# Performance work log

Measured on AMD Instinct MI355X. Metric: run time of the kernel, lower is better.

## Reference

```python
import jax, jax.numpy as jnp
import numpy as np

NUM_ORI = 16
DEGREE = 2
NUM_LAYERS = 2
LN_EPS = 1e-6


def ori_grid_s1(n):
    theta = jnp.linspace(0.0, 2.0 * jnp.pi, n + 1)[:-1]
    return jnp.stack([jnp.cos(theta), jnp.sin(theta)], axis=-1)  # (O, 2)


def poly_feats(z, degree):
    # PolynomialFeatures: [z, z*z outer, (z*z)*z outer ...] flattened
    feats = [z]
    p = z
    for _ in range(degree):
        p = (p[..., :, None] * z[..., None, :]).reshape(*z.shape[:-1], -1)
        feats.append(p)
    return jnp.concatenate(feats, axis=-1)


def basis_mlp(z, W1, b1, W2, b2):
    return jax.nn.gelu(jax.nn.gelu(z @ W1 + b1) @ W2 + b2)


def layer_norm(h, scale, bias):
    mu = h.mean(axis=-1, keepdims=True)
    var = ((h - mu) ** 2).mean(axis=-1, keepdims=True)
    return (h - mu) * jax.lax.rsqrt(var + LN_EPS) * scale + bias


def setup_inputs() -> dict:
    key = jax.random.key(0)
    ks = jax.random.split(key, 16)
    B, N, NIN, H, BD, WF, OUT, L = 1, 256, 3, 64, 32, 4, 3, NUM_LAYERS
    s = 0.05
    return {
        'pos': jax.random.normal(ks[0], (B, N, 2), jnp.float32),
        'x': jax.random.normal(ks[1], (B, N, NIN), jnp.float32),
        'skb_W1': jax.random.normal(ks[2], (14, H), jnp.float32) * s,
        'skb_b1': jnp.zeros((H,), jnp.float32),
        'skb_W2': jax.random.normal(ks[3], (H, BD), jnp.float32) * s,
        'skb_b2': jnp.zeros((BD,), jnp.float32),
        'rkb_W1': jax.random.normal(ks[4], (3, H), jnp.float32) * s,
        'rkb_b1': jnp.zeros((H,), jnp.float32),
        'rkb_W2': jax.random.normal(ks[5], (H, BD), jnp.float32) * s,
        'rkb_b2': jnp.zeros((BD,), jnp.float32),
        'emb_W': jax.random.normal(ks[6], (NIN, H), jnp.float32) * s,
        'conv_sW': jax.random.normal(ks[7], (L, BD, H), jnp.float32) * s,
        'conv_rW': jax.random.normal(ks[8], (L, BD, H), jnp.float32) * s,
        'conv_b': jnp.zeros((L, H), jnp.float32),
        'ln_scale': jnp.ones((L, H), jnp.float32),
        'ln_bias': jnp.zeros((L, H), jnp.float32),
        'lin1_W': jax.random.normal(ks[9], (L, H, WF * H), jnp.float32) * s,
        'lin1_b': jnp.zeros((L, WF * H), jnp.float32),
        'lin2_W': jax.random.normal(ks[10], (L, WF * H, H), jnp.float32) * s,
        'lin2_b': jnp.zeros((L, H), jnp.float32),
        'readout_W': jax.random.normal(ks[11], (H, OUT), jnp.float32) * s,
    }


def reference(pos, x, skb_W1, skb_b1, skb_W2, skb_b2, rkb_W1, rkb_b1, rkb_W2, rkb_b2,
              emb_W, conv_sW, conv_rW, conv_b, ln_scale, ln_bias,
              lin1_W, lin1_b, lin2_W, lin2_b, readout_W):
    ori = ori_grid_s1(NUM_ORI)  # (O, 2)
    # rel_pos: (B, n, m, 1, 2) -> broadcast against ori (O, 2)
    rel_pos = pos[:, None, :, None, :] - pos[:, :, None, None, :]
    inv1 = jnp.sum(rel_pos * ori[None, None, None, :, :], axis=-1, keepdims=True)  # (B,N,N,O,1)
    inv2 = jnp.linalg.norm(rel_pos - rel_pos * inv1, axis=-1, keepdims=True)       # (B,N,N,O,1)
    spatial_inv = jnp.concatenate([inv1, inv2], axis=-1)                            # (B,N,N,O,2)
    orient_inv = jnp.sum(ori[:, None, :] * ori[None, :, :], axis=-1, keepdims=True) # (O,O,1)

    kernel_basis = basis_mlp(poly_feats(spatial_inv, DEGREE), skb_W1, skb_b1, skb_W2, skb_b2)  # (B,N,N,O,BD)
    fiber_basis = basis_mlp(poly_feats(orient_inv, DEGREE), rkb_W1, rkb_b1, rkb_W2, rkb_b2)    # (O,O,BD)

    h = x @ emb_W                                  # (B,N,H)
    O = NUM_ORI
    h = jnp.broadcast_to(h[:, :, None, :], (h.shape[0], h.shape[1], O, h.shape[2]))  # (B,N,O,H)

    for i in range(NUM_LAYERS):
        inp = h
        sk = kernel_basis @ conv_sW[i]             # (B,N,N,O,H)
        rk = fiber_basis @ conv_rW[i]              # (O,O,H)
        c = jnp.einsum('bnoc,bmnoc->bmoc', h, sk)  # spatial aggregation
        c = jnp.einsum('bmoc,poc->bmpc', c, rk)    # orientation mixing
        c = c + conv_b[i]
        c = layer_norm(c, ln_scale[i], ln_bias[i])
        c = jax.nn.gelu(c @ lin1_W[i] + lin1_b[i]) @ lin2_W[i] + lin2_b[i]
        h = inp + c

    readout = h @ readout_W                        # (B,N,O,OUT)
    out_scalar = readout.mean(axis=-2)             # (B,N,OUT)
    out_scalar = jnp.sum(out_scalar, axis=1) / out_scalar.shape[1]  # global pool -> (B,OUT)
    return out_scalar
```

## Files before the change

kernel.cpp:

```cpp
#include <hip/hip_runtime.h>
#include <math.h>

#define NPTS 256
#define NORI 16
#define CH   64
#define BD   32
#define HID  64
#define STEP16 0.39269908169872414f

typedef __bf16 bf16x8 __attribute__((ext_vector_type(8)));
typedef float  f32x4  __attribute__((ext_vector_type(4)));

#define MFMA16(a, b, cc) __builtin_amdgcn_mfma_f32_16x16x32_bf16(a, b, cc, 0, 0, 0)

__device__ __forceinline__ float gelu_f(float x) {
    float x2 = x * x;
    float y2 = x * fmaf(0.07135481627f, x2, 1.5957691216f);
    float e = __expf(y2);
    return x - x * __builtin_amdgcn_rcpf(e + 1.0f);
}

__device__ __forceinline__ unsigned pk2(float x, float y) {
    union { __bf16 h[2]; unsigned u; } r;
    r.h[0] = (__bf16)x; r.h[1] = (__bf16)y;
    return r.u;
}

__device__ __forceinline__ void dev_prep(
    const float* __restrict__ skb_W1, const float* __restrict__ skb_W2,
    const float* __restrict__ conv_sW,
    __bf16* __restrict__ w1T, __bf16* __restrict__ w2T, __bf16* __restrict__ w2Tlo,
    __bf16* __restrict__ sWT, __bf16* __restrict__ sWTlo, int t)
{
    if (t < 64) {
        float f[9];
        f[0] = skb_W1[t];
        f[1] = skb_W1[64 + t];
        f[2] = skb_W1[128 + t];
        f[3] = skb_W1[192 + t] + skb_W1[256 + t];
        f[4] = skb_W1[320 + t];
        f[5] = skb_W1[384 + t];
        f[6] = skb_W1[448 + t] + skb_W1[512 + t] + skb_W1[640 + t];
        f[7] = skb_W1[576 + t] + skb_W1[704 + t] + skb_W1[768 + t];
        f[8] = skb_W1[832 + t];
#pragma unroll
        for (int k = 0; k < 9; ++k) {
            __bf16 hi = (__bf16)f[k];
            w1T[t * 32 + k]      = hi;
            w1T[t * 32 + 9 + k]  = (__bf16)(f[k] - (float)hi);
            w1T[t * 32 + 18 + k] = hi;
        }
#pragma unroll
        for (int k = 27; k < 32; ++k) w1T[t * 32 + k] = (__bf16)0.0f;
    }
    for (int i = t; i < 2048; i += 256) {
        int n = i >> 6, kk = i & 63;
        float v = skb_W2[kk * 32 + n];
        __bf16 hi = (__bf16)v;
        w2T[i]   = hi;
        w2Tlo[i] = (__bf16)(v - (float)hi);
    }
    for (int i = t; i < 4096; i += 256) {
        int ll = i >> 11, chh = (i >> 5) & 63, k = i & 31;
        float v = conv_sW[(ll * 32 + k) * 64 + chh];
        __bf16 hi = (__bf16)v;
        sWT[i]   = hi;
        sWTlo[i] = (__bf16)(v - (float)hi);
    }
}

__device__ __forceinline__ void dev_fiber(
    const float* __restrict__ rkb_W1, const float* __restrict__ rkb_b1,
    const float* __restrict__ rkb_W2, const float* __restrict__ rkb_b2,
    const float* __restrict__ conv_rW, float* __restrict__ rk, int p, int t)
{
    __shared__ float w1L[3 * 64], b1L[64], w2L[64 * 32], b2L[32];
    __shared__ float rwL[2 * 32 * 64];
    __shared__ float t1L[16 * 64];
    __shared__ float fbL[16 * 32];

    if (t < 192) w1L[t] = rkb_W1[t];
    if (t >= 192 && t < 256) b1L[t - 192] = rkb_b1[t - 192];
    for (int i = t; i < 2048; i += 256) w2L[i] = rkb_W2[i];
    if (t < 32) b2L[t] = rkb_b2[t];
    for (int i = t; i < 4096; i += 256) rwL[i] = conv_rW[i];
    __syncthreads();

    const int o = t & 15;
    const float cp = cosf(p * STEP16), sp = sinf(p * STEP16);
    const float co = cosf(o * STEP16), so = sinf(o * STEP16);
    const float s0 = cp * co + sp * so;
    const float m1 = s0 * s0, m2 = m1 * s0;

    {
        const int jg = t >> 4;
#pragma unroll
        for (int u = 0; u < 4; ++u) {
            const int j = jg * 4 + u;
            float a = b1L[j] + s0 * w1L[j] + m1 * w1L[64 + j] + m2 * w1L[128 + j];
            t1L[o * 64 + j] = gelu_f(a);
        }
    }
    __syncthreads();
    {
        const int kg = t >> 4;
#pragma unroll
        for (int kk = 0; kk < 2; ++kk) {
            const int k = kg + kk * 16;
            float a = b2L[k];
#pragma unroll
            for (int j = 0; j < 64; ++j) a += t1L[o * 64 + j] * w2L[j * 32 + k];
            fbL[o * 32 + k] = gelu_f(a);
        }
    }
    __syncthreads();
    {
        const int o2 = t >> 4;
        const int chg = (t & 15) * 4;
#pragma unroll
        for (int l = 0; l < 2; ++l) {
            f32x4 acc = {0.f, 0.f, 0.f, 0.f};
#pragma unroll
            for (int k = 0; k < 32; ++k) {
                const float fv = fbL[o2 * 32 + k];
                const f32x4 rv = *(const f32x4*)(rwL + (l * 32 + k) * 64 + chg);
                acc[0] = fmaf(fv, rv[0], acc[0]);
                acc[1] = fmaf(fv, rv[1], acc[1]);
                acc[2] = fmaf(fv, rv[2], acc[2]);
                acc[3] = fmaf(fv, rv[3], acc[3]);
            }
            *(f32x4*)(rk + (l * 256 + p * 16 + o2) * 64 + chg) = acc;
        }
    }
}

__global__ __launch_bounds__(256) void k_prep(
    const float* __restrict__ skb_W1, const float* __restrict__ skb_W2,
    const float* __restrict__ conv_sW,
    __bf16* __restrict__ w1T, __bf16* __restrict__ w2T, __bf16* __restrict__ w2Tlo,
    __bf16* __restrict__ sWT, __bf16* __restrict__ sWTlo)
{
    dev_prep(skb_W1, skb_W2, conv_sW, w1T, w2T, w2Tlo, sWT, sWTlo, threadIdx.x);
}

__global__ __launch_bounds__(256) void k_fiber2(
    const float* __restrict__ rkb_W1, const float* __restrict__ rkb_b1,
    const float* __restrict__ rkb_W2, const float* __restrict__ rkb_b2,
    const float* __restrict__ conv_rW, float* __restrict__ rk)
{
    dev_fiber(rkb_W1, rkb_b1, rkb_W2, rkb_b2, conv_rW, rk, blockIdx.x, threadIdx.x);
}

__global__ __launch_bounds__(256) void k_init(
    const float* __restrict__ x, const float* __restrict__ emb_W, float* __restrict__ h)
{
    int idx = blockIdx.x * 256 + threadIdx.x;
    int ch = idx & 63;
    int n  = idx >> 10;
    h[idx] = x[n * 3] * emb_W[ch] + x[n * 3 + 1] * emb_W[64 + ch] + x[n * 3 + 2] * emb_W[128 + ch];
}

__global__ __launch_bounds__(256) void k_setup(
    const float* __restrict__ x, const float* __restrict__ emb_W, float* __restrict__ h2,
    const float* __restrict__ rkb_W1, const float* __restrict__ rkb_b1,
    const float* __restrict__ rkb_W2, const float* __restrict__ rkb_b2,
    const float* __restrict__ conv_rW, float* __restrict__ rk,
    const float* __restrict__ skb_W1, const float* __restrict__ skb_W2,
    const float* __restrict__ conv_sW,
    __bf16* __restrict__ w1T, __bf16* __restrict__ w2T, __bf16* __restrict__ w2Tlo,
    __bf16* __restrict__ sWT, __bf16* __restrict__ sWTlo)
{
    const int b = blockIdx.x, t = threadIdx.x;
    if (b < 1024) {
        int idx = b * 256 + t;
        int ch = (idx >> 4) & 63;
        int n  = idx >> 10;
        h2[idx] = x[n * 3] * emb_W[ch] + x[n * 3 + 1] * emb_W[64 + ch]
                + x[n * 3 + 2] * emb_W[128 + ch];
    } else if (b < 1040) {
        dev_fiber(rkb_W1, rkb_b1, rkb_W2, rkb_b2, conv_rW, rk, b - 1024, t);
    } else {
        dev_prep(skb_W1, skb_W2, conv_sW, w1T, w2T, w2Tlo, sWT, sWTlo, t);
    }
}

__global__ __launch_bounds__(256) void k_kb2(
    const float* __restrict__ pos,
    const float* __restrict__ skb_b1, const float* __restrict__ skb_b2,
    const __bf16* __restrict__ w1T, const __bf16* __restrict__ w2T,
    const __bf16* __restrict__ w2Tlo, __bf16* __restrict__ kb_g)
{
    const int t = threadIdx.x;
    const int c = t & 15, qq = (t >> 4) & 3, w = t >> 6;
    const int pair = blockIdx.x >> 1, ohalf = blockIdx.x & 1;
    const int m0 = (pair >> 4) * 16, n0 = (pair & 15) * 16;

    bf16x8 w1B[4], w2A[2][2], w2Alo[2][2];
    float b1x[4][4], b2x[2][4];
#pragma unroll
    for (int ni = 0; ni < 4; ++ni) {
        w1B[ni] = *(const bf16x8*)(w1T + (ni * 16 + c) * 32 + qq * 8);
#pragma unroll
        for (int r = 0; r < 4; ++r) b1x[ni][r] = skb_b1[ni * 16 + qq * 4 + r];
    }
#pragma unroll
    for (int mk = 0; mk < 2; ++mk) {
#pragma unroll
        for (int ks = 0; ks < 2; ++ks) {
            w2A[mk][ks]   = *(const bf16x8*)(w2T   + (mk * 16 + c) * 64 + ks * 32 + qq * 8);
            w2Alo[mk][ks] = *(const bf16x8*)(w2Tlo + (mk * 16 + c) * 64 + ks * 32 + qq * 8);
        }
#pragma unroll
        for (int r = 0; r < 4; ++r) b2x[mk][r] = skb_b2[mk * 16 + qq * 4 + r];
    }

    const int n = n0 + c;
    const float pnx = pos[2 * n], pny = pos[2 * n + 1];
    float cosv[4], sinv[4];
#pragma unroll
    for (int oi = 0; oi < 4; ++oi) {
        float th = (float)(ohalf * 4 + oi) * STEP16;
        cosv[oi] = cosf(th); sinv[oi] = sinf(th);
    }
    const int s0lane = c + ((qq & 1) << 5);
    const int s1lane = s0lane + 16;
    const int selhi = qq >> 1;
    const f32x4 zf = {0.f, 0.f, 0.f, 0.f};

#pragma unroll 1
    for (int mi = 0; mi < 4; ++mi) {
        const int m = m0 + w * 4 + mi;
        const float dx = pnx - pos[2 * m];
        const float dy = pny - pos[2 * m + 1];
#pragma unroll
        for (int oi = 0; oi < 4; ++oi) {
            const int o = ohalf * 4 + oi;
            float a = dx * cosv[oi] + dy * sinv[oi];
            float vx = dx - dx * a, vy = dy - dy * a;
            float b = sqrtf(vx * vx + vy * vy);
            float mfv[9];
            mfv[0] = a; mfv[1] = b; mfv[2] = a * a; mfv[3] = a * b; mfv[4] = b * b;
            mfv[5] = mfv[2] * a; mfv[6] = mfv[2] * b; mfv[7] = mfv[3] * b; mfv[8] = mfv[4] * b;
            __bf16 mh[9], ml[9];
#pragma unroll
            for (int i = 0; i < 9; ++i) {
                mh[i] = (__bf16)mfv[i];
                ml[i] = (__bf16)(mfv[i] - (float)mh[i]);
            }
            bf16x8 mb;
            if (qq == 0) {
                mb[0]=mh[0]; mb[1]=mh[1]; mb[2]=mh[2]; mb[3]=mh[3];
                mb[4]=mh[4]; mb[5]=mh[5]; mb[6]=mh[6]; mb[7]=mh[7];
            } else if (qq == 1) {
                mb[0]=mh[8]; mb[1]=mh[0]; mb[2]=mh[1]; mb[3]=mh[2];
                mb[4]=mh[3]; mb[5]=mh[4]; mb[6]=mh[5]; mb[7]=mh[6];
            } else if (qq == 2) {
                mb[0]=mh[7]; mb[1]=mh[8]; mb[2]=ml[0]; mb[3]=ml[1];
                mb[4]=ml[2]; mb[5]=ml[3]; mb[6]=ml[4]; mb[7]=ml[5];
            } else {
                mb[0]=ml[6]; mb[1]=ml[7]; mb[2]=ml[8]; mb[3]=(__bf16)0.0f;
                mb[4]=(__bf16)0.0f; mb[5]=(__bf16)0.0f; mb[6]=(__bf16)0.0f; mb[7]=(__bf16)0.0f;
            }

            unsigned t1p[4][2];
#pragma unroll
            for (int ni = 0; ni < 4; ++ni) {
                f32x4 acc = MFMA16(w1B[ni], mb, zf);
                float g0 = gelu_f(acc[0] + b1x[ni][0]);
                float g1 = gelu_f(acc[1] + b1x[ni][1]);
                float g2 = gelu_f(acc[2] + b1x[ni][2]);
                float g3 = gelu_f(acc[3] + b1x[ni][3]);
                t1p[ni][0] = pk2(g0, g1);
                t1p[ni][1] = pk2(g2, g3);
            }

            bf16x8 B2[2];
#pragma unroll
            for (int ks = 0; ks < 2; ++ks) {
                const unsigned lo0 = t1p[ks * 2][0],     lo1 = t1p[ks * 2][1];
                const unsigned hi0 = t1p[ks * 2 + 1][0], hi1 = t1p[ks * 2 + 1][1];
                unsigned aL0 = (unsigned)__shfl((int)lo0, s0lane);
                unsigned aL1 = (unsigned)__shfl((int)lo1, s0lane);
                unsigned aL2 = (unsigned)__shfl((int)lo0, s1lane);
                unsigned aL3 = (unsigned)__shfl((int)lo1, s1lane);
                unsigned aH0 = (unsigned)__shfl((int)hi0, s0lane);
                unsigned aH1 = (unsigned)__shfl((int)hi1, s0lane);
                unsigned aH2 = (unsigned)__shfl((int)hi0, s1lane);
                unsigned aH3 = (unsigned)__shfl((int)hi1, s1lane);
                union { unsigned u[4]; bf16x8 v; } bu;
                bu.u[0] = selhi ? aH0 : aL0;
                bu.u[1] = selhi ? aH1 : aL1;
                bu.u[2] = selhi ? aH2 : aL2;
                bu.u[3] = selhi ? aH3 : aL3;
                B2[ks] = bu.v;
            }

            const size_t ptP = (size_t)((m * 256 + n) * 16 + o);
            const size_t ptM = (size_t)((n * 256 + m) * 16 + (o ^ 8));
#pragma unroll
            for (int mk = 0; mk < 2; ++mk) {
                f32x4 acc = MFMA16(w2A[mk][0], B2[0], zf);
                acc = MFMA16(w2A[mk][1], B2[1], acc);
                acc = MFMA16(w2Alo[mk][0], B2[0], acc);
                acc = MFMA16(w2Alo[mk][1], B2[1], acc);
                float g0 = gelu_f(acc[0] + b2x[mk][0]);
                float g1 = gelu_f(acc[1] + b2x[mk][1]);
                float g2 = gelu_f(acc[2] + b2x[mk][2]);
                float g3 = gelu_f(acc[3] + b2x[mk][3]);
                uint2 pv; pv.x = pk2(g0, g1); pv.y = pk2(g2, g3);
                const int off = mk * 32 + qq * 8;
                *(uint2*)((char*)kb_g + ptP * 64 + off) = pv;
                *(uint2*)((char*)kb_g + ptM * 64 + off) = pv;
            }
        }
    }
}

__global__ __launch_bounds__(512, 1) void k_conv(
    const __bf16* __restrict__ kb_g,
    const __bf16* __restrict__ sWT, const __bf16* __restrict__ sWTlo,
    const float* __restrict__ conv_b, const float* __restrict__ rkg,
    const float* __restrict__ ln_scale, const float* __restrict__ ln_bias,
    const float* __restrict__ lin1_W, const float* __restrict__ lin1_b,
    const float* __restrict__ lin2_W, const float* __restrict__ lin2_b,
    const float* __restrict__ h_in, float* __restrict__ h_out, int l)
{
    __shared__ __align__(16) unsigned char smem[57344];
    const int t = threadIdx.x;
    const int m = blockIdx.x;
    const int w = t >> 6, lane = t & 63;
    const int qq = lane >> 4, c = lane & 15;

    bf16x8 sWB[4], sWBlo[4];
#pragma unroll
    for (int ni = 0; ni < 4; ++ni) {
        sWB[ni]   = *(const bf16x8*)(sWT   + l * 2048 + (ni * 16 + c) * 32 + qq * 8);
        sWBlo[ni] = *(const bf16x8*)(sWTlo + l * 2048 + (ni * 16 + c) * 32 + qq * 8);
    }

    f32x4 cacc[4];
#pragma unroll
    for (int ni = 0; ni < 4; ++ni)
#pragma unroll
        for (int r = 0; r < 4; ++r) cacc[ni][r] = 0.f;

    const __bf16* kbm = kb_g + ((size_t)m << 17);

#pragma unroll 2
    for (int tile = 0; tile < 16; ++tile) {
#pragma unroll
        for (int mm = 0; mm < 2; ++mm) {
            const int mi = 2 * w + mm;
            const int n = tile * 16 + mi;
            bf16x8 aF = *(const bf16x8*)(kbm + (size_t)(tile * 256 + mi * 16 + c) * 32 + qq * 8);
#pragma unroll
            for (int ni = 0; ni < 4; ++ni) {
                f32x4 g3 = {0.f, 0.f, 0.f, 0.f};
                g3 = MFMA16(aF, sWB[ni], g3);
                g3 = MFMA16(aF, sWBlo[ni], g3);
                f32x4 hv = *(const f32x4*)(h_in + n * 1024 + (ni * 16 + c) * 16 + qq * 4);
#pragma unroll
                for (int r = 0; r < 4; ++r) cacc[ni][r] = fmaf(g3[r], hv[r], cacc[ni][r]);
            }
        }
    }

    {
        float* c1p = (float*)smem;
#pragma unroll
        for (int ni = 0; ni < 4; ++ni)
#pragma unroll
            for (int r = 0; r < 4; ++r)
                c1p[w * 1024 + (qq * 4 + r) * 64 + ni * 16 + c] = cacc[ni][r];
    }
    __syncthreads();
    {
        float* c1p = (float*)smem;
        float* c1r = (float*)(smem + 32768);
        for (int i = t; i < 1024; i += 512) {
            float s = 0.f;
#pragma unroll
            for (int ww = 0; ww < 8; ++ww) s += c1p[ww * 1024 + i];
            c1r[i] = s;
        }
    }
    __syncthreads();

    {
        float* c1r = (float*)(smem + 32768);
        float* cns = (float*)(smem + 36864);
        const int ch = lane;
        const float cb  = conv_b[l * 64 + ch];
        const float lsc = ln_scale[l * 64 + ch], lbi = ln_bias[l * 64 + ch];
#pragma unroll
        for (int pp = 0; pp < 2; ++pp) {
            const int p = w + pp * 8;
            const float* rkp = rkg + (l * 256 + p * 16) * 64 + ch;
            float s = cb;
#pragma unroll
            for (int o = 0; o < 16; ++o) s += c1r[o * 64 + ch] * rkp[o * 64];
            float red = s;
#pragma unroll
            for (int off = 32; off > 0; off >>= 1) red += __shfl_xor(red, off);
            float mu = red * (1.0f / 64.0f);
            float d = s - mu;
            float r2 = d * d;
#pragma unroll
            for (int off = 32; off > 0; off >>= 1) r2 += __shfl_xor(r2, off);
            cns[p * 64 + ch] = d * rsqrtf(r2 * (1.0f / 64.0f) + 1e-6f) * lsc + lbi;
        }
    }
    __syncthreads();

    {
        float* cns = (float*)(smem + 36864);
        float* usS = (float*)(smem + 40960);
        const int j = t & 255, half = t >> 8;
        const float* W1l = lin1_W + l * 64 * 256;
        const float bl1 = lin1_b[l * 256 + j];
        float ua[8];
#pragma unroll
        for (int pi = 0; pi < 8; ++pi) ua[pi] = bl1;
#pragma unroll 4
        for (int c2 = 0; c2 < 64; ++c2) {
            const float wv = W1l[c2 * 256 + j];
#pragma unroll
            for (int pi = 0; pi < 8; ++pi)
                ua[pi] = fmaf(cns[(half * 8 + pi) * 64 + c2], wv, ua[pi]);
        }
#pragma unroll
        for (int pi = 0; pi < 8; ++pi) usS[(half * 8 + pi) * 256 + j] = gelu_f(ua[pi]);
    }
    __syncthreads();

    {
        float* usS = (float*)(smem + 40960);
        const int ch2 = t & 63, pg = t >> 6;
        const float* W2l = lin2_W + l * 256 * 64;
        const float bl2 = lin2_b[l * 64 + ch2];
        float o0 = bl2, o1 = bl2;
#pragma unroll 4
        for (int j = 0; j < 256; ++j) {
            const float wv = W2l[j * 64 + ch2];
            o0 = fmaf(usS[pg * 256 + j], wv, o0);
            o1 = fmaf(usS[(pg + 8) * 256 + j], wv, o1);
        }
        const int i0 = m * 1024 + ch2 * 16 + pg;
        h_out[i0]     = h_in[i0]     + o0;
        h_out[i0 + 8] = h_in[i0 + 8] + o1;
    }
}

__global__ __launch_bounds__(512, 1) void k_layer2(
    const float* __restrict__ pos,
    const float* __restrict__ skb_b1, const float* __restrict__ skb_b2,
    const __bf16* __restrict__ w1T, const __bf16* __restrict__ w2T,
    const __bf16* __restrict__ w2Tlo,
    const __bf16* __restrict__ sWT, const __bf16* __restrict__ sWTlo,
    const float* __restrict__ conv_b, const float* __restrict__ rkg,
    const float* __restrict__ ln_scale, const float* __restrict__ ln_bias,
    const float* __restrict__ lin1_W, const float* __restrict__ lin1_b,
    const float* __restrict__ lin2_W, const float* __restrict__ lin2_b,
    const float* __restrict__ h_in, float* __restrict__ h_out, int l)
{
    __shared__ __align__(16) unsigned char smem[57344];
    const int t = threadIdx.x;
    const int m = blockIdx.x;
    const int w = t >> 6, lane = t & 63;
    const int qq = lane >> 4, c = lane & 15;

    bf16x8 w1B[4], sWB[4], sWBlo[4], w2B[2][2], w2Blo[2][2];
    float b1v[4], b2v[2];
#pragma unroll
    for (int ni = 0; ni < 4; ++ni) {
        w1B[ni]   = *(const bf16x8*)(w1T + (ni * 16 + c) * 32 + qq * 8);
        sWB[ni]   = *(const bf16x8*)(sWT   + l * 2048 + (ni * 16 + c) * 32 + qq * 8);
        sWBlo[ni] = *(const bf16x8*)(sWTlo + l * 2048 + (ni * 16 + c) * 32 + qq * 8);
        b1v[ni] = skb_b1[ni * 16 + c];
    }
#pragma unroll
    for (int nt = 0; nt < 2; ++nt) {
        b2v[nt] = skb_b2[nt * 16 + c];
#pragma unroll
        for (int ks = 0; ks < 2; ++ks) {
            w2B[nt][ks]   = *(const bf16x8*)(w2T   + (nt * 16 + c) * 64 + ks * 32 + qq * 8);
            w2Blo[nt][ks] = *(const bf16x8*)(w2Tlo + (nt * 16 + c) * 64 + ks * 32 + qq * 8);
        }
    }

    const float pmx = pos[2 * m], pmy = pos[2 * m + 1];
    float co_ = 0.f, so_ = 0.f;
    if (t < 256) { float th = (float)(t & 15) * STEP16; co_ = cosf(th); so_ = sinf(th); }

    f32x4 cacc[4];
#pragma unroll
    for (int ni = 0; ni < 4; ++ni)
#pragma unroll
        for (int r = 0; r < 4; ++r) cacc[ni][r] = 0.f;

#pragma unroll 1
    for (int tile = 0; tile < 16; ++tile) {
        if (t < 256) {
            const int n = tile * 16 + (t >> 4);
            float dx = pos[2 * n] - pmx, dy = pos[2 * n + 1] - pmy;
            float a = dx * co_ + dy * so_;
            float vx = dx - dx * a, vy = dy - dy * a;
            float b = sqrtf(vx * vx + vy * vy);
            float mf[9];
            mf[0] = a; mf[1] = b; mf[2] = a * a; mf[3] = a * b; mf[4] = b * b;
            mf[5] = mf[2] * a; mf[6] = mf[2] * b; mf[7] = mf[3] * b; mf[8] = mf[4] * b;
            __bf16 s[32];
#pragma unroll
            for (int i = 0; i < 9; ++i) {
                __bf16 hi = (__bf16)mf[i];
                s[i] = hi; s[9 + i] = hi;
                s[18 + i] = (__bf16)(mf[i] - (float)hi);
            }
#pragma unroll
            for (int i = 27; i < 32; ++i) s[i] = (__bf16)0.0f;
            unsigned char* rowp = smem + t * 64;
#pragma unroll
            for (int u = 0; u < 4; ++u) {
                bf16x8 vv;
#pragma unroll
                for (int j = 0; j < 8; ++j) vv[j] = s[u * 8 + j];
                *(bf16x8*)(rowp + ((u ^ (t & 3)) << 4)) = vv;
            }
        }
        __syncthreads();

#pragma unroll
        for (int mm = 0; mm < 2; ++mm) {
            const int row = (2 * w + mm) * 16 + c;
            bf16x8 aF = *(const bf16x8*)(smem + row * 64 + ((qq ^ (row & 3)) << 4));
#pragma unroll
            for (int ni = 0; ni < 4; ++ni) {
                f32x4 acc = {0.f, 0.f, 0.f, 0.f};
                acc = MFMA16(aF, w1B[ni], acc);
#pragma unroll
                for (int r = 0; r < 4; ++r) {
                    const int ro = (2 * w + mm) * 16 + qq * 4 + r;
                    float g = gelu_f(acc[r] + b1v[ni]);
                    const int chc = ni * 16 + c;
                    *(__bf16*)(smem + 16384 + ro * 128 + (((chc >> 3) ^ (ro & 7)) << 4)
                               + ((chc & 7) << 1)) = (__bf16)g;
                }
            }
        }
        __syncthreads();

#pragma unroll
        for (int mm = 0; mm < 2; ++mm) {
            const int row = (2 * w + mm) * 16 + c;
            bf16x8 a0 = *(const bf16x8*)(smem + 16384 + row * 128 + ((qq ^ (row & 7)) << 4));
            bf16x8 a1 = *(const bf16x8*)(smem + 16384 + row * 128 + (((4 + qq) ^ (row & 7)) << 4));
#pragma unroll
            for (int nt = 0; nt < 2; ++nt) {
                f32x4 acc = {0.f, 0.f, 0.f, 0.f};
                acc = MFMA16(a0, w2B[nt][0], acc);
                acc = MFMA16(a1, w2B[nt][1], acc);
                acc = MFMA16(a0, w2Blo[nt][0], acc);
                acc = MFMA16(a1, w2Blo[nt][1], acc);
#pragma unroll
                for (int r = 0; r < 4; ++r) {
                    const int ro = (2 * w + mm) * 16 + qq * 4 + r;
                    float g = gelu_f(acc[r] + b2v[nt]);
                    const int kc = nt * 16 + c;
                    *(__bf16*)(smem + ro * 64 + (((kc >> 3) ^ (ro & 3)) << 4)
                               + ((kc & 7) << 1)) = (__bf16)g;
                }
            }
        }
        __syncthreads();

#pragma unroll
        for (int mm = 0; mm < 2; ++mm) {
            const int mi = 2 * w + mm;
            const int row = mi * 16 + c;
            bf16x8 aF = *(const bf16x8*)(smem + row * 64 + ((qq ^ (row & 3)) << 4));
            const int nbase = (tile * 16 + mi) * 1024 + qq * 256;
#pragma unroll
            for (int ni = 0; ni < 4; ++ni) {
                f32x4 g3 = {0.f, 0.f, 0.f, 0.f};
                g3 = MFMA16(aF, sWB[ni], g3);
                g3 = MFMA16(aF, sWBlo[ni], g3);
#pragma unroll
                for (int r = 0; r < 4; ++r) {
                    float hv = h_in[nbase + r * 64 + ni * 16 + c];
                    cacc[ni][r] = fmaf(g3[r], hv, cacc[ni][r]);
                }
            }
        }
        __syncthreads();
    }

    {
        float* c1p = (float*)smem;
#pragma unroll
        for (int ni = 0; ni < 4; ++ni)
#pragma unroll
            for (int r = 0; r < 4; ++r)
                c1p[w * 1024 + (qq * 4 + r) * 64 + ni * 16 + c] = cacc[ni][r];
    }
    __syncthreads();
    {
        float* c1p = (float*)smem;
        float* c1r = (float*)(smem + 32768);
        for (int i = t; i < 1024; i += 512) {
            float s = 0.f;
#pragma unroll
            for (int ww = 0; ww < 8; ++ww) s += c1p[ww * 1024 + i];
            c1r[i] = s;
        }
    }
    __syncthreads();

    {
        float* c1r = (float*)(smem + 32768);
        float* cns = (float*)(smem + 36864);
        const int ch = lane;
        const float cb  = conv_b[l * 64 + ch];
        const float lsc = ln_scale[l * 64 + ch], lbi = ln_bias[l * 64 + ch];
#pragma unroll
        for (int pp = 0; pp < 2; ++pp) {
            const int p = w + pp * 8;
            const float* rkp = rkg + (l * 256 + p * 16) * 64 + ch;
            float s = cb;
#pragma unroll
            for (int o = 0; o < 16; ++o) s += c1r[o * 64 + ch] * rkp[o * 64];
            float red = s;
#pragma unroll
            for (int off = 32; off > 0; off >>= 1) red += __shfl_xor(red, off);
            float mu = red * (1.0f / 64.0f);
            float d = s - mu;
            float r2 = d * d;
#pragma unroll
            for (int off = 32; off > 0; off >>= 1) r2 += __shfl_xor(r2, off);
            cns[p * 64 + ch] = d * rsqrtf(r2 * (1.0f / 64.0f) + 1e-6f) * lsc + lbi;
        }
    }
    __syncthreads();

    {
        float* cns = (float*)(smem + 36864);
        float* usS = (float*)(smem + 40960);
        const int j = t & 255, half = t >> 8;
        const float* W1l = lin1_W + l * 64 * 256;
        const float bl1 = lin1_b[l * 256 + j];
        float ua[8];
#pragma unroll
        for (int pi = 0; pi < 8; ++pi) ua[pi] = bl1;
#pragma unroll 1
        for (int c2 = 0; c2 < 64; ++c2) {
            const float wv = W1l[c2 * 256 + j];
#pragma unroll
            for (int pi = 0; pi < 8; ++pi)
                ua[pi] = fmaf(cns[(half * 8 + pi) * 64 + c2], wv, ua[pi]);
        }
#pragma unroll
        for (int pi = 0; pi < 8; ++pi) usS[(half * 8 + pi) * 256 + j] = gelu_f(ua[pi]);
    }
    __syncthreads();

    {
        float* usS = (float*)(smem + 40960);
        const int ch2 = t & 63, pg = t >> 6;
        const float* W2l = lin2_W + l * 256 * 64;
        const float bl2 = lin2_b[l * 64 + ch2];
        float o0 = bl2, o1 = bl2;
#pragma unroll 2
        for (int j = 0; j < 256; ++j) {
            const float wv = W2l[j * 64 + ch2];
            o0 = fmaf(usS[pg * 256 + j], wv, o0);
            o1 = fmaf(usS[(pg + 8) * 256 + j], wv, o1);
        }
        const int i0 = (m * 16 + pg) * 64 + ch2;
        const int i1 = (m * 16 + pg + 8) * 64 + ch2;
        h_out[i0] = h_in[i0] + o0;
        h_out[i1] = h_in[i1] + o1;
    }
}

__global__ __launch_bounds__(256) void k_readout_part(
    const float* __restrict__ h, float* __restrict__ part16)
{
    __shared__ float part[4][64];
    const int t = threadIdx.x, b = blockIdx.x;
    const int c = t & 63, seg = t >> 6;
    float s = 0.f;
    const int r0 = b * 256 + seg * 64;
    for (int r = r0; r < r0 + 64; ++r) s += h[r * 64 + c];
    part[seg][c] = s;
    __syncthreads();
    if (t < 64) part16[b * 64 + t] = part[0][t] + part[1][t] + part[2][t] + part[3][t];
}

__global__ __launch_bounds__(256) void k_readout_part2(
    const float* __restrict__ h, float* __restrict__ part16)
{
    const int t = threadIdx.x, b = blockIdx.x;
    const int ch = t >> 2, oq = t & 3;
    float s = 0.f;
#pragma unroll
    for (int nn = 0; nn < 16; ++nn) {
        const int n = b * 16 + nn;
        f32x4 v = *(const f32x4*)(h + n * 1024 + ch * 16 + oq * 4);
        s += (v[0] + v[1]) + (v[2] + v[3]);
    }
    s += __shfl_xor(s, 1);
    s += __shfl_xor(s, 2);
    if (oq == 0) part16[b * 64 + ch] = s;
}

__global__ __launch_bounds__(64) void k_readout_final(
    const float* __restrict__ part16, const float* __restrict__ rW, float* __restrict__ out)
{
    __shared__ float hbar[64];
    const int t = threadIdx.x;
    float s = 0.f;
#pragma unroll
    for (int b = 0; b < 16; ++b) s += part16[b * 64 + t];
    hbar[t] = s * (1.0f / 4096.0f);
    __syncthreads();
    if (t < 3) {
        float s2 = 0.f;
#pragma unroll
        for (int k = 0; k < 64; ++k) s2 += hbar[k] * rW[k * 3 + t];
        out[t] = s2;
    }
}

extern "C" void kernel_launch(void* const* d_in, const int* in_sizes, int n_in,
                              void* d_out, int out_size, void* d_ws, size_t ws_size,
                              hipStream_t stream)
{
    const float* pos      = (const float*)d_in[0];
    const float* x        = (const float*)d_in[1];
    const float* skb_W1   = (const float*)d_in[2];
    const float* skb_b1   = (const float*)d_in[3];
    const float* skb_W2   = (const float*)d_in[4];
    const float* skb_b2   = (const float*)d_in[5];
    const float* rkb_W1   = (const float*)d_in[6];
    const float* rkb_b1   = (const float*)d_in[7];
    const float* rkb_W2   = (const float*)d_in[8];
    const float* rkb_b2   = (const float*)d_in[9];
    const float* emb_W    = (const float*)d_in[10];
    const float* conv_sW  = (const float*)d_in[11];
    const float* conv_rW  = (const float*)d_in[12];
    const float* conv_b   = (const float*)d_in[13];
    const float* ln_scale = (const float*)d_in[14];
    const float* ln_bias  = (const float*)d_in[15];
    const float* lin1_W   = (const float*)d_in[16];
    const float* lin1_b   = (const float*)d_in[17];
    const float* lin2_W   = (const float*)d_in[18];
    const float* lin2_b   = (const float*)d_in[19];
    const float* readout_W= (const float*)d_in[20];
    float* out = (float*)d_out;

    unsigned char* ws = (unsigned char*)d_ws;
    float*  h_a    = (float*)(ws);
    float*  h_b    = (float*)(ws + 1048576);
    float*  rkw    = (float*)(ws + 2097152);
    __bf16* w1T    = (__bf16*)(ws + 2228224);
    __bf16* w2T    = (__bf16*)(ws + 2232320);
    __bf16* w2Tlo  = (__bf16*)(ws + 2236416);
    __bf16* sWT    = (__bf16*)(ws + 2240512);
    __bf16* sWTlo  = (__bf16*)(ws + 2248704);
    float*  part16 = (float*)(ws + 2256896);
    __bf16* kb_g   = (__bf16*)(ws + 2260992);

    const bool fast = (ws_size >= 2260992ull + 67108864ull);

    if (fast) {
        k_setup<<<1041, 256, 0, stream>>>(x, emb_W, h_a,
                                          rkb_W1, rkb_b1, rkb_W2, rkb_b2, conv_rW, rkw,
                                          skb_W1, skb_W2, conv_sW,
                                          w1T, w2T, w2Tlo, sWT, sWTlo);
        k_kb2<<<512, 256, 0, stream>>>(pos, skb_b1, skb_b2, w1T, w2T, w2Tlo, kb_g);
        k_conv<<<256, 512, 0, stream>>>(kb_g, sWT, sWTlo, conv_b, rkw,
                                        ln_scale, ln_bias, lin1_W, lin1_b,
                                        lin2_W, lin2_b, h_a, h_b, 0);
        k_conv<<<256, 512, 0, stream>>>(kb_g, sWT, sWTlo, conv_b, rkw,
                                        ln_scale, ln_bias, lin1_W, lin1_b,
                                        lin2_W, lin2_b, h_b, h_a, 1);
        k_readout_part2<<<16, 256, 0, stream>>>(h_a, part16);
        k_readout_final<<<1, 64, 0, stream>>>(part16, readout_W, out);
    } else {
        k_prep<<<1, 256, 0, stream>>>(skb_W1, skb_W2, conv_sW, w1T, w2T, w2Tlo, sWT, sWTlo);
        k_fiber2<<<16, 256, 0, stream>>>(rkb_W1, rkb_b1, rkb_W2, rkb_b2, conv_rW, rkw);
        k_init<<<1024, 256, 0, stream>>>(x, emb_W, h_a);
        k_layer2<<<256, 512, 0, stream>>>(pos, skb_b1, skb_b2, w1T, w2T, w2Tlo, sWT, sWTlo,
                                          conv_b, rkw, ln_scale, ln_bias, lin1_W, lin1_b,
                                          lin2_W, lin2_b, h_a, h_b, 0);
        k_layer2<<<256, 512, 0, stream>>>(pos, skb_b1, skb_b2, w1T, w2T, w2Tlo, sWT, sWTlo,
                                          conv_b, rkw, ln_scale, ln_bias, lin1_W, lin1_b,
                                          lin2_W, lin2_b, h_b, h_a, 1);
        k_readout_part<<<16, 256, 0, stream>>>(h_a, part16);
        k_readout_final<<<1, 64, 0, stream>>>(part16, readout_W, out);
    }
}
```

Before: 157.2 us.

## Halve kernel-basis storage via symmetry, split conv into partial-sum and epilogue kernels

The kernel-basis precompute now stores only half of the orientations (8 instead of 16) per (m,n) pair with an XOR-swizzled chunk layout. The conv kernel reconstructs the mirrored half by reading the transposed (n,m) entry. The kernel-basis launch is spread over four times as many blocks, each handling one m row. The conv is split into a parallel partial-sum kernel (512 blocks, two m rows by a quarter of the n range) and a separate epilogue kernel that reduces the partials and runs layernorm plus the MLP. This cuts kernel-basis memory traffic and raises parallelism, at the cost of extra launches and a partial-sum buffer round trip through global memory.

```diff
diff --git a/kernel.cpp b/kernel.cpp
--- a/kernel.cpp
+++ b/kernel.cpp
@@ -192,7 +192,11 @@
 {
     const int t = threadIdx.x;
     const int c = t & 15, qq = (t >> 4) & 3, w = t >> 6;
-    const int pair = blockIdx.x >> 1, ohalf = blockIdx.x & 1;
+    const int b = blockIdx.x;
+    const int pair = b >> 3;
+    const int ohalf = (b >> 2) & 1;
+    const int mhalf = (b >> 1) & 1;
+    const int mi2   = b & 1;
     const int m0 = (pair >> 4) * 16, n0 = (pair & 15) * 16;
 
     bf16x8 w1B[4], w2A[2][2], w2Alo[2][2];
@@ -227,168 +231,205 @@
     const int selhi = qq >> 1;
     const f32x4 zf = {0.f, 0.f, 0.f, 0.f};
 
-#pragma unroll 1
-    for (int mi = 0; mi < 4; ++mi) {
-        const int m = m0 + w * 4 + mi;
-        const float dx = pnx - pos[2 * m];
-        const float dy = pny - pos[2 * m + 1];
-#pragma unroll
-        for (int oi = 0; oi < 4; ++oi) {
-            const int o = ohalf * 4 + oi;
-            float a = dx * cosv[oi] + dy * sinv[oi];
-            float vx = dx - dx * a, vy = dy - dy * a;
-            float b = sqrtf(vx * vx + vy * vy);
-            float mfv[9];
-            mfv[0] = a; mfv[1] = b; mfv[2] = a * a; mfv[3] = a * b; mfv[4] = b * b;
-            mfv[5] = mfv[2] * a; mfv[6] = mfv[2] * b; mfv[7] = mfv[3] * b; mfv[8] = mfv[4] * b;
-            __bf16 mh[9], ml[9];
-#pragma unroll
-            for (int i = 0; i < 9; ++i) {
-                mh[i] = (__bf16)mfv[i];
-                ml[i] = (__bf16)(mfv[i] - (float)mh[i]);
-            }
-            bf16x8 mb;
-            if (qq == 0) {
-                mb[0]=mh[0]; mb[1]=mh[1]; mb[2]=mh[2]; mb[3]=mh[3];
-                mb[4]=mh[4]; mb[5]=mh[5]; mb[6]=mh[6]; mb[7]=mh[7];
-            } else if (qq == 1) {
-                mb[0]=mh[8]; mb[1]=mh[0]; mb[2]=mh[1]; mb[3]=mh[2];
-                mb[4]=mh[3]; mb[5]=mh[4]; mb[6]=mh[5]; mb[7]=mh[6];
-            } else if (qq == 2) {
-                mb[0]=mh[7]; mb[1]=mh[8]; mb[2]=ml[0]; mb[3]=ml[1];
-                mb[4]=ml[2]; mb[5]=ml[3]; mb[6]=ml[4]; mb[7]=ml[5];
-            } else {
-                mb[0]=ml[6]; mb[1]=ml[7]; mb[2]=ml[8]; mb[3]=(__bf16)0.0f;
-                mb[4]=(__bf16)0.0f; mb[5]=(__bf16)0.0f; mb[6]=(__bf16)0.0f; mb[7]=(__bf16)0.0f;
-            }
-
-            unsigned t1p[4][2];
-#pragma unroll
-            for (int ni = 0; ni < 4; ++ni) {
-                f32x4 acc = MFMA16(w1B[ni], mb, zf);
-                float g0 = gelu_f(acc[0] + b1x[ni][0]);
-                float g1 = gelu_f(acc[1] + b1x[ni][1]);
-                float g2 = gelu_f(acc[2] + b1x[ni][2]);
-                float g3 = gelu_f(acc[3] + b1x[ni][3]);
-                t1p[ni][0] = pk2(g0, g1);
-                t1p[ni][1] = pk2(g2, g3);
-            }
-
-            bf16x8 B2[2];
-#pragma unroll
-            for (int ks = 0; ks < 2; ++ks) {
-                const unsigned lo0 = t1p[ks * 2][0],     lo1 = t1p[ks * 2][1];
-                const unsigned hi0 = t1p[ks * 2 + 1][0], hi1 = t1p[ks * 2 + 1][1];
-                unsigned aL0 = (unsigned)__shfl((int)lo0, s0lane);
-                unsigned aL1 = (unsigned)__shfl((int)lo1, s0lane);
-                unsigned aL2 = (unsigned)__shfl((int)lo0, s1lane);
-                unsigned aL3 = (unsigned)__shfl((int)lo1, s1lane);
-                unsigned aH0 = (unsigned)__shfl((int)hi0, s0lane);
-                unsigned aH1 = (unsigned)__shfl((int)hi1, s0lane);
-                unsigned aH2 = (unsigned)__shfl((int)hi0, s1lane);
-                unsigned aH3 = (unsigned)__shfl((int)hi1, s1lane);
-                union { unsigned u[4]; bf16x8 v; } bu;
-                bu.u[0] = selhi ? aH0 : aL0;
-                bu.u[1] = selhi ? aH1 : aL1;
-                bu.u[2] = selhi ? aH2 : aL2;
-                bu.u[3] = selhi ? aH3 : aL3;
-                B2[ks] = bu.v;
-            }
-
-            const size_t ptP = (size_t)((m * 256 + n) * 16 + o);
-            const size_t ptM = (size_t)((n * 256 + m) * 16 + (o ^ 8));
-#pragma unroll
-            for (int mk = 0; mk < 2; ++mk) {
-                f32x4 acc = MFMA16(w2A[mk][0], B2[0], zf);
-                acc = MFMA16(w2A[mk][1], B2[1], acc);
-                acc = MFMA16(w2Alo[mk][0], B2[0], acc);
-                acc = MFMA16(w2Alo[mk][1], B2[1], acc);
-                float g0 = gelu_f(acc[0] + b2x[mk][0]);
-                float g1 = gelu_f(acc[1] + b2x[mk][1]);
-                float g2 = gelu_f(acc[2] + b2x[mk][2]);
-                float g3 = gelu_f(acc[3] + b2x[mk][3]);
-                uint2 pv; pv.x = pk2(g0, g1); pv.y = pk2(g2, g3);
-                const int off = mk * 32 + qq * 8;
-                *(uint2*)((char*)kb_g + ptP * 64 + off) = pv;
-                *(uint2*)((char*)kb_g + ptM * 64 + off) = pv;
-            }
-        }
-    }
-}
-
-__global__ __launch_bounds__(512, 1) void k_conv(
+    const int m = m0 + w * 4 + mhalf * 2 + mi2;
+    const float dx = pnx - pos[2 * m];
+    const float dy = pny - pos[2 * m + 1];
+#pragma unroll
+    for (int oi = 0; oi < 4; ++oi) {
+        const int o = ohalf * 4 + oi;
+        float a = dx * cosv[oi] + dy * sinv[oi];
+        float vx = dx - dx * a, vy = dy - dy * a;
+        float b2 = sqrtf(vx * vx + vy * vy);
+        float mfv[9];
+        mfv[0] = a; mfv[1] = b2; mfv[2] = a * a; mfv[3] = a * b2; mfv[4] = b2 * b2;
+        mfv[5] = mfv[2] * a; mfv[6] = mfv[2] * b2; mfv[7] = mfv[3] * b2; mfv[8] = mfv[4] * b2;
+        __bf16 mh[9], ml[9];
+#pragma unroll
+        for (int i = 0; i < 9; ++i) {
+            mh[i] = (__bf16)mfv[i];
+            ml[i] = (__bf16)(mfv[i] - (float)mh[i]);
+        }
+        bf16x8 mb;
+        if (qq == 0) {
+            mb[0]=mh[0]; mb[1]=mh[1]; mb[2]=mh[2]; mb[3]=mh[3];
+            mb[4]=mh[4]; mb[5]=mh[5]; mb[6]=mh[6]; mb[7]=mh[7];
+        } else if (qq == 1) {
+            mb[0]=mh[8]; mb[1]=mh[0]; mb[2]=mh[1]; mb[3]=mh[2];
+            mb[4]=mh[3]; mb[5]=mh[4]; mb[6]=mh[5]; mb[7]=mh[6];
+        } else if (qq == 2) {
+            mb[0]=mh[7]; mb[1]=mh[8]; mb[2]=ml[0]; mb[3]=ml[1];
+            mb[4]=ml[2]; mb[5]=ml[3]; mb[6]=ml[4]; mb[7]=ml[5];
+        } else {
+            mb[0]=ml[6]; mb[1]=ml[7]; mb[2]=ml[8]; mb[3]=(__bf16)0.0f;
+            mb[4]=(__bf16)0.0f; mb[5]=(__bf16)0.0f; mb[6]=(__bf16)0.0f; mb[7]=(__bf16)0.0f;
+        }
+
+        unsigned t1p[4][2];
+#pragma unroll
+        for (int ni = 0; ni < 4; ++ni) {
+            f32x4 acc = MFMA16(w1B[ni], mb, zf);
+            float g0 = gelu_f(acc[0] + b1x[ni][0]);
+            float g1 = gelu_f(acc[1] + b1x[ni][1]);
+            float g2 = gelu_f(acc[2] + b1x[ni][2]);
+            float g3 = gelu_f(acc[3] + b1x[ni][3]);
+            t1p[ni][0] = pk2(g0, g1);
+            t1p[ni][1] = pk2(g2, g3);
+        }
+
+        bf16x8 B2[2];
+#pragma unroll
+        for (int ks = 0; ks < 2; ++ks) {
+            const unsigned lo0 = t1p[ks * 2][0],     lo1 = t1p[ks * 2][1];
+            const unsigned hi0 = t1p[ks * 2 + 1][0], hi1 = t1p[ks * 2 + 1][1];
+            unsigned aL0 = (unsigned)__shfl((int)lo0, s0lane);
+            unsigned aL1 = (unsigned)__shfl((int)lo1, s0lane);
+            unsigned aL2 = (unsigned)__shfl((int)lo0, s1lane);
+            unsigned aL3 = (unsigned)__shfl((int)lo1, s1lane);
+            unsigned aH0 = (unsigned)__shfl((int)hi0, s0lane);
+            unsigned aH1 = (unsigned)__shfl((int)hi1, s0lane);
+            unsigned aH2 = (unsigned)__shfl((int)hi0, s1lane);
+            unsigned aH3 = (unsigned)__shfl((int)hi1, s1lane);
+            union { unsigned u[4]; bf16x8 v; } bu;
+            bu.u[0] = selhi ? aH0 : aL0;
+            bu.u[1] = selhi ? aH1 : aL1;
+            bu.u[2] = selhi ? aH2 : aL2;
+            bu.u[3] = selhi ? aH3 : aL3;
+            B2[ks] = bu.v;
+        }
+
+        const size_t ptP = (size_t)(m * 256 + n) * 8 + o;
+        const int swz = o & 3;
+#pragma unroll
+        for (int mk = 0; mk < 2; ++mk) {
+            f32x4 acc = MFMA16(w2A[mk][0], B2[0], zf);
+            acc = MFMA16(w2A[mk][1], B2[1], acc);
+            acc = MFMA16(w2Alo[mk][0], B2[0], acc);
+            acc = MFMA16(w2Alo[mk][1], B2[1], acc);
+            float g0 = gelu_f(acc[0] + b2x[mk][0]);
+            float g1 = gelu_f(acc[1] + b2x[mk][1]);
+            float g2 = gelu_f(acc[2] + b2x[mk][2]);
+            float g3 = gelu_f(acc[3] + b2x[mk][3]);
+            uint2 pv; pv.x = pk2(g0, g1); pv.y = pk2(g2, g3);
+            const int off = (((mk * 2 + (qq >> 1)) ^ swz) << 4) + ((qq & 1) << 3);
+            *(uint2*)((char*)kb_g + ptP * 64 + off) = pv;
+        }
+    }
+}
+
+__global__ __launch_bounds__(512) void k_conv10(
     const __bf16* __restrict__ kb_g,
     const __bf16* __restrict__ sWT, const __bf16* __restrict__ sWTlo,
+    const float* __restrict__ h_in, float* __restrict__ c1part, int l)
+{
+    __shared__ __align__(16) float c1p[16 * 1024];
+    const int t = threadIdx.x;
+    const int mg = blockIdx.x >> 2, q = blockIdx.x & 3;
+    const int m0 = 2 * mg, m1 = 2 * mg + 1;
+    const int w = t >> 6, lane = t & 63;
+    const int qq = lane >> 4, c = lane & 15;
+    const f32x4 zf = {0.f, 0.f, 0.f, 0.f};
+
+    bf16x8 sWB[4], sWBlo[4];
+#pragma unroll
+    for (int ni = 0; ni < 4; ++ni) {
+        sWB[ni]   = *(const bf16x8*)(sWT   + l * 2048 + (ni * 16 + c) * 32 + qq * 8);
+        sWBlo[ni] = *(const bf16x8*)(sWTlo + l * 2048 + (ni * 16 + c) * 32 + qq * 8);
+    }
+
+    f32x4 cacc0[4], cacc1[4];
+#pragma unroll
+    for (int ni = 0; ni < 4; ++ni) { cacc0[ni] = zf; cacc1[ni] = zf; }
+
+    const int chunk = (qq ^ (c & 3)) << 4;
+    const char* kbb = (const char*)kb_g;
+
+#pragma unroll
+    for (int step = 0; step < 8; ++step) {
+        const int n = q * 64 + step * 8 + w;
+        const float* hp = h_in + n * 1024 + c * 16 + qq * 4;
+        f32x4 hv0 = *(const f32x4*)(hp);
+        f32x4 hv1 = *(const f32x4*)(hp + 256);
+        f32x4 hv2 = *(const f32x4*)(hp + 512);
+        f32x4 hv3 = *(const f32x4*)(hp + 768);
+        size_t lp0, lp1;
+        if (c < 8) { lp0 = (size_t)m0 * 2048 + (size_t)n * 8 + c;
+                     lp1 = (size_t)m1 * 2048 + (size_t)n * 8 + c; }
+        else       { lp0 = (size_t)n * 2048 + (size_t)m0 * 8 + (c - 8);
+                     lp1 = (size_t)n * 2048 + (size_t)m1 * 8 + (c - 8); }
+        bf16x8 a0 = *(const bf16x8*)(kbb + lp0 * 64 + chunk);
+        bf16x8 a1 = *(const bf16x8*)(kbb + lp1 * 64 + chunk);
+
+        f32x4 g;
+        g = MFMA16(a0, sWB[0], zf);  g = MFMA16(a0, sWBlo[0], g);
+#pragma unroll
+        for (int r = 0; r < 4; ++r) cacc0[0][r] = fmaf(g[r], hv0[r], cacc0[0][r]);
+        g = MFMA16(a0, sWB[1], zf);  g = MFMA16(a0, sWBlo[1], g);
+#pragma unroll
+        for (int r = 0; r < 4; ++r) cacc0[1][r] = fmaf(g[r], hv1[r], cacc0[1][r]);
+        g = MFMA16(a0, sWB[2], zf);  g = MFMA16(a0, sWBlo[2], g);
+#pragma unroll
+        for (int r = 0; r < 4; ++r) cacc0[2][r] = fmaf(g[r], hv2[r], cacc0[2][r]);
+        g = MFMA16(a0, sWB[3], zf);  g = MFMA16(a0, sWBlo[3], g);
+#pragma unroll
+        for (int r = 0; r < 4; ++r) cacc0[3][r] = fmaf(g[r], hv3[r], cacc0[3][r]);
+
+        g = MFMA16(a1, sWB[0], zf);  g = MFMA16(a1, sWBlo[0], g);
+#pragma unroll
+        for (int r = 0; r < 4; ++r) cacc1[0][r] = fmaf(g[r], hv0[r], cacc1[0][r]);
+        g = MFMA16(a1, sWB[1], zf);  g = MFMA16(a1, sWBlo[1], g);
+#pragma unroll
+        for (int r = 0; r < 4; ++r) cacc1[1][r] = fmaf(g[r], hv1[r], cacc1[1][r]);
+        g = MFMA16(a1, sWB[2], zf);  g = MFMA16(a1, sWBlo[2], g);
+#pragma unroll
+        for (int r = 0; r < 4; ++r) cacc1[2][r] = fmaf(g[r], hv2[r], cacc1[2][r]);
+        g = MFMA16(a1, sWB[3], zf);  g = MFMA16(a1, sWBlo[3], g);
+#pragma unroll
+        for (int r = 0; r < 4; ++r) cacc1[3][r] = fmaf(g[r], hv3[r], cacc1[3][r]);
+    }
+
+#pragma unroll
+    for (int ni = 0; ni < 4; ++ni)
+#pragma unroll
+        for (int r = 0; r < 4; ++r) {
+            c1p[(w * 2 + 0) * 1024 + (qq * 4 + r) * 64 + ni * 16 + c] = cacc0[ni][r];
+            c1p[(w * 2 + 1) * 1024 + (qq * 4 + r) * 64 + ni * 16 + c] = cacc1[ni][r];
+        }
+    __syncthreads();
+    for (int i = t; i < 1024; i += 512) {
+        float s0 = 0.f, s1 = 0.f;
+#pragma unroll
+        for (int ww = 0; ww < 8; ++ww) {
+            s0 += c1p[(ww * 2 + 0) * 1024 + i];
+            s1 += c1p[(ww * 2 + 1) * 1024 + i];
+        }
+        c1part[((size_t)q * 256 + m0) * 1024 + i] = s0;
+        c1part[((size_t)q * 256 + m1) * 1024 + i] = s1;
+    }
+}
+
+__global__ __launch_bounds__(512) void k_convepi10(
+    const float* __restrict__ c1part,
     const float* __restrict__ conv_b, const float* __restrict__ rkg,
     const float* __restrict__ ln_scale, const float* __restrict__ ln_bias,
     const float* __restrict__ lin1_W, const float* __restrict__ lin1_b,
     const float* __restrict__ lin2_W, const float* __restrict__ lin2_b,
     const float* __restrict__ h_in, float* __restrict__ h_out, int l)
 {
-    __shared__ __align__(16) unsigned char smem[57344];
+    __shared__ float c1r[1024];
+    __shared__ float cns[1024];
+    __shared__ float usS[4096];
     const int t = threadIdx.x;
     const int m = blockIdx.x;
     const int w = t >> 6, lane = t & 63;
-    const int qq = lane >> 4, c = lane & 15;
-
-    bf16x8 sWB[4], sWBlo[4];
-#pragma unroll
-    for (int ni = 0; ni < 4; ++ni) {
-        sWB[ni]   = *(const bf16x8*)(sWT   + l * 2048 + (ni * 16 + c) * 32 + qq * 8);
-        sWBlo[ni] = *(const bf16x8*)(sWTlo + l * 2048 + (ni * 16 + c) * 32 + qq * 8);
-    }
-
-    f32x4 cacc[4];
-#pragma unroll
-    for (int ni = 0; ni < 4; ++ni)
-#pragma unroll
-        for (int r = 0; r < 4; ++r) cacc[ni][r] = 0.f;
-
-    const __bf16* kbm = kb_g + ((size_t)m << 17);
-
-#pragma unroll 2
-    for (int tile = 0; tile < 16; ++tile) {
-#pragma unroll
-        for (int mm = 0; mm < 2; ++mm) {
-            const int mi = 2 * w + mm;
-            const int n = tile * 16 + mi;
-            bf16x8 aF = *(const bf16x8*)(kbm + (size_t)(tile * 256 + mi * 16 + c) * 32 + qq * 8);
-#pragma unroll
-            for (int ni = 0; ni < 4; ++ni) {
-                f32x4 g3 = {0.f, 0.f, 0.f, 0.f};
-                g3 = MFMA16(aF, sWB[ni], g3);
-                g3 = MFMA16(aF, sWBlo[ni], g3);
-                f32x4 hv = *(const f32x4*)(h_in + n * 1024 + (ni * 16 + c) * 16 + qq * 4);
-#pragma unroll
-                for (int r = 0; r < 4; ++r) cacc[ni][r] = fmaf(g3[r], hv[r], cacc[ni][r]);
-            }
-        }
-    }
-
-    {
-        float* c1p = (float*)smem;
-#pragma unroll
-        for (int ni = 0; ni < 4; ++ni)
-#pragma unroll
-            for (int r = 0; r < 4; ++r)
-                c1p[w * 1024 + (qq * 4 + r) * 64 + ni * 16 + c] = cacc[ni][r];
-    }
-    __syncthreads();
-    {
-        float* c1p = (float*)smem;
-        float* c1r = (float*)(smem + 32768);
-        for (int i = t; i < 1024; i += 512) {
-            float s = 0.f;
-#pragma unroll
-            for (int ww = 0; ww < 8; ++ww) s += c1p[ww * 1024 + i];
-            c1r[i] = s;
-        }
-    }
-    __syncthreads();
-
-    {
-        float* c1r = (float*)(smem + 32768);
-        float* cns = (float*)(smem + 36864);
+
+    for (int i = t; i < 1024; i += 512)
+        c1r[i] = c1part[((size_t)0 * 256 + m) * 1024 + i]
+               + c1part[((size_t)1 * 256 + m) * 1024 + i]
+               + c1part[((size_t)2 * 256 + m) * 1024 + i]
+               + c1part[((size_t)3 * 256 + m) * 1024 + i];
+    __syncthreads();
+
+    {
         const int ch = lane;
         const float cb  = conv_b[l * 64 + ch];
         const float lsc = ln_scale[l * 64 + ch], lbi = ln_bias[l * 64 + ch];
@@ -413,9 +454,7 @@
     __syncthreads();
 
     {
-        float* cns = (float*)(smem + 36864);
-        float* usS = (float*)(smem + 40960);
-        const int j = t & 255, half = t >> 8;
+        const int j = t & 255, hf = t >> 8;
         const float* W1l = lin1_W + l * 64 * 256;
         const float bl1 = lin1_b[l * 256 + j];
         float ua[8];
@@ -426,15 +465,14 @@
             const float wv = W1l[c2 * 256 + j];
 #pragma unroll
             for (int pi = 0; pi < 8; ++pi)
-                ua[pi] = fmaf(cns[(half * 8 + pi) * 64 + c2], wv, ua[pi]);
-        }
-#pragma unroll
-        for (int pi = 0; pi < 8; ++pi) usS[(half * 8 + pi) * 256 + j] = gelu_f(ua[pi]);
-    }
-    __syncthreads();
-
-    {
-        float* usS = (float*)(smem + 40960);
+                ua[pi] = fmaf(cns[(hf * 8 + pi) * 64 + c2], wv, ua[pi]);
+        }
+#pragma unroll
+        for (int pi = 0; pi < 8; ++pi) usS[(hf * 8 + pi) * 256 + j] = gelu_f(ua[pi]);
+    }
+    __syncthreads();
+
+    {
         const int ch2 = t & 63, pg = t >> 6;
         const float* W2l = lin2_W + l * 256 * 64;
         const float bl2 = lin2_b[l * 64 + ch2];
@@ -768,21 +806,22 @@
     __bf16* sWTlo  = (__bf16*)(ws + 2248704);
     float*  part16 = (float*)(ws + 2256896);
     __bf16* kb_g   = (__bf16*)(ws + 2260992);
-
-    const bool fast = (ws_size >= 2260992ull + 67108864ull);
+    float*  c1part = (float*)(ws + 35815424);
+
+    const bool fast = (ws_size >= 40009728ull);
 
     if (fast) {
         k_setup<<<1041, 256, 0, stream>>>(x, emb_W, h_a,
                                           rkb_W1, rkb_b1, rkb_W2, rkb_b2, conv_rW, rkw,
                                           skb_W1, skb_W2, conv_sW,
                                           w1T, w2T, w2Tlo, sWT, sWTlo);
-        k_kb2<<<512, 256, 0, stream>>>(pos, skb_b1, skb_b2, w1T, w2T, w2Tlo, kb_g);
-        k_conv<<<256, 512, 0, stream>>>(kb_g, sWT, sWTlo, conv_b, rkw,
-                                        ln_scale, ln_bias, lin1_W, lin1_b,
-                                        lin2_W, lin2_b, h_a, h_b, 0);
-        k_conv<<<256, 512, 0, stream>>>(kb_g, sWT, sWTlo, conv_b, rkw,
-                                        ln_scale, ln_bias, lin1_W, lin1_b,
-                                        lin2_W, lin2_b, h_b, h_a, 1);
+        k_kb2<<<2048, 256, 0, stream>>>(pos, skb_b1, skb_b2, w1T, w2T, w2Tlo, kb_g);
+        k_conv10<<<512, 512, 0, stream>>>(kb_g, sWT, sWTlo, h_a, c1part, 0);
+        k_convepi10<<<256, 512, 0, stream>>>(c1part, conv_b, rkw, ln_scale, ln_bias,
+                                             lin1_W, lin1_b, lin2_W, lin2_b, h_a, h_b, 0);
+        k_conv10<<<512, 512, 0, stream>>>(kb_g, sWT, sWTlo, h_b, c1part, 1);
+        k_convepi10<<<256, 512, 0, stream>>>(c1part, conv_b, rkw, ln_scale, ln_bias,
+                                             lin1_W, lin1_b, lin2_W, lin2_b, h_b, h_a, 1);
         k_readout_part2<<<16, 256, 0, stream>>>(h_a, part16);
         k_readout_final<<<1, 64, 0, stream>>>(part16, readout_W, out);
     } else {
```

Measured after the change: 237.7 us. 1.51x slower.
